# Performance work log

Measured on AMD Instinct MI355X. Metric: run time of the kernel, lower is better.

Reference implementation:

```python
import jax, jax.numpy as jnp
import numpy as np

B, T, D, H = 2, 2048, 1024, 16
DH = D // H
EPS = 1e-3  # keras LayerNormalization default epsilon


def setup_inputs() -> dict:
    key = jax.random.key(0)
    ks = jax.random.split(key, 10)
    s = 1.0 / np.sqrt(D)
    return {
        "x": jax.random.normal(ks[0], (B, T, D), jnp.float32),
        "wq": jax.random.normal(ks[1], (D, D), jnp.float32) * s,
        "bq": jnp.zeros((D,), jnp.float32),
        "wk": jax.random.normal(ks[2], (D, D), jnp.float32) * s,
        "bk": jnp.zeros((D,), jnp.float32),
        "wv": jax.random.normal(ks[3], (D, D), jnp.float32) * s,
        "bv": jnp.zeros((D,), jnp.float32),
        "wo": jax.random.normal(ks[4], (D, D), jnp.float32) * s,
        "bo": jnp.zeros((D,), jnp.float32),
        "scale": jnp.asarray(1.0, jnp.float32),  # learnable scalar, init 1.0
        "gamma": jnp.ones((D,), jnp.float32),
        "beta": jnp.zeros((D,), jnp.float32),
    }


def _split_heads(t):
    # [B,T,D] -> [B,T,H,DH] -> [H,B,T,DH]; head h takes channels h*DH:(h+1)*DH,
    # matching tf.concat(tf.split(t, H, axis=-1), axis=0) up to batch layout.
    return t.reshape(B, T, H, DH).transpose(2, 0, 1, 3)


def reference(x, wq, bq, wk, bk, wv, bv, wo, bo, scale, gamma, beta):
    q = _split_heads(x @ wq + bq)  # [H,B,T,DH]
    k = _split_heads(x @ wk + bk)
    v = _split_heads(x @ wv + bv)
    scores = scale * jnp.einsum("hbqd,hbkd->hbqk", q, k)  # [H,B,Tq,Tk]
    attn = jax.nn.softmax(scores, axis=-1)
    ctx = jnp.einsum("hbqk,hbkd->hbqd", attn, v)  # [H,B,T,DH]
    # inverse of split: heads back to last dim in head order
    merged = ctx.transpose(1, 2, 0, 3).reshape(B, T, D)
    out = merged @ wo + bo
    out = out + x  # residual connection
    mean = jnp.mean(out, axis=-1, keepdims=True)
    var = jnp.var(out, axis=-1, keepdims=True)
    out = (out - mean) * jax.lax.rsqrt(var + EPS) * gamma + beta
    return out
```

## Files before the change

kernel.cpp:

```cpp
#include <hip/hip_runtime.h>
#include <hip/hip_bf16.h>

#define B_ 2
#define T_ 2048
#define D_ 1024
#define H_ 16
#define M_ (B_ * T_)

typedef __attribute__((ext_vector_type(4))) float f32x4;
typedef __attribute__((ext_vector_type(16))) float f32x16;
typedef __attribute__((ext_vector_type(8))) short s16x8;
typedef __attribute__((ext_vector_type(4))) short s16x4;
typedef __attribute__((ext_vector_type(4))) unsigned u32x4;

__device__ __forceinline__ short f2bs(float f) {
  unsigned u = __builtin_bit_cast(unsigned, f);
  u += 0x7fffu + ((u >> 16) & 1u);
  return (short)(u >> 16);
}
__device__ __forceinline__ unsigned cvt_pk_bf16(float lo, float hi) {
  unsigned r;
  asm("v_cvt_pk_bf16_f32 %0, %1, %2" : "=v"(r) : "v"(lo), "v"(hi));
  return r;
}

__global__ __launch_bounds__(256) void cvt_f32_bf16(const float* __restrict__ in,
                                                    short* __restrict__ out, int n4) {
  int i = blockIdx.x * 256 + threadIdx.x;
  if (i < n4) {
    float4 v = ((const float4*)in)[i];
    s16x4 o;
    o.x = f2bs(v.x); o.y = f2bs(v.y); o.z = f2bs(v.z); o.w = f2bs(v.w);
    ((s16x4*)out)[i] = o;
  }
}

__global__ __launch_bounds__(256) void cvt_transpose(
    const float* __restrict__ w0, const float* __restrict__ w1,
    const float* __restrict__ w2, const float* __restrict__ w3,
    short* __restrict__ o0, short* __restrict__ o1,
    short* __restrict__ o2, short* __restrict__ o3) {
  __shared__ float tile[64][65];
  const float* W; short* Wt;
  if (blockIdx.z == 0) { W = w0; Wt = o0; }
  else if (blockIdx.z == 1) { W = w1; Wt = o1; }
  else if (blockIdx.z == 2) { W = w2; Wt = o2; }
  else { W = w3; Wt = o3; }
  const int k0 = blockIdx.x * 64, n0 = blockIdx.y * 64;
  const int t = threadIdx.x;
  const int c = t & 63, r4 = t >> 6;
#pragma unroll
  for (int i = 0; i < 16; ++i) {
    int row = i * 4 + r4;
    tile[row][c] = W[(size_t)(k0 + row) * D_ + n0 + c];
  }
  __syncthreads();
#pragma unroll
  for (int i = 0; i < 16; ++i) {
    int row = i * 4 + r4;
    Wt[(size_t)(n0 + row) * D_ + k0 + c] = f2bs(tile[c][row]);
  }
}

template <int MODE>
__device__ __forceinline__ void gemm_core(short As[128][72], short Bs[128][72],
                                          const short* __restrict__ A,
                                          const short* __restrict__ Wt,
                                          const float* __restrict__ bias,
                                          const float* __restrict__ resid,
                                          void* __restrict__ outp, float mult) {
  const int t = threadIdx.x;
  const int lane = t & 63, wid = t >> 6;
  const int l15 = lane & 15, g = lane >> 4;
  const int wr = wid >> 1, wc = wid & 1;
  const int f = blockIdx.y * 8 + blockIdx.x;
  const int nf = (f & 7) * 32 + (f >> 3);
  const int n0 = (nf & 7) * 128;
  const int m0 = (nf >> 3) * 128;

  const f32x4 fz = {0.f, 0.f, 0.f, 0.f};
  f32x4 acc[4][4];
#pragma unroll
  for (int m = 0; m < 4; ++m)
#pragma unroll
    for (int n = 0; n < 4; ++n) acc[m][n] = fz;

  const int srow = t >> 1, shalf = (t & 1) * 32;
  const short* ap = A + (size_t)(m0 + srow) * D_ + shalf;
  const short* bp = Wt + (size_t)(n0 + srow) * D_ + shalf;

  s16x8 ar[4], br[4];
#pragma unroll
  for (int c = 0; c < 4; ++c) {
    ar[c] = *(const s16x8*)(ap + c * 8);
    br[c] = *(const s16x8*)(bp + c * 8);
  }

  for (int k0 = 0; k0 < D_; k0 += 64) {
    __syncthreads();
#pragma unroll
    for (int c = 0; c < 4; ++c) {
      *(s16x8*)&As[srow][shalf + c * 8] = ar[c];
      *(s16x8*)&Bs[srow][shalf + c * 8] = br[c];
    }
    __syncthreads();
    if (k0 + 64 < D_) {
#pragma unroll
      for (int c = 0; c < 4; ++c) {
        ar[c] = *(const s16x8*)(ap + k0 + 64 + c * 8);
        br[c] = *(const s16x8*)(bp + k0 + 64 + c * 8);
      }
    }
#pragma unroll
    for (int kk = 0; kk < 64; kk += 32) {
      s16x8 af[4], bfr[4];
#pragma unroll
      for (int m = 0; m < 4; ++m)
        af[m] = *(const s16x8*)&As[wr * 64 + m * 16 + l15][kk + g * 8];
#pragma unroll
      for (int n = 0; n < 4; ++n)
        bfr[n] = *(const s16x8*)&Bs[wc * 64 + n * 16 + l15][kk + g * 8];
#pragma unroll
      for (int m = 0; m < 4; ++m)
#pragma unroll
        for (int n = 0; n < 4; ++n)
          acc[m][n] = __builtin_amdgcn_mfma_f32_16x16x32_bf16(af[m], bfr[n], acc[m][n], 0, 0, 0);
    }
  }

#pragma unroll
  for (int m = 0; m < 4; ++m) {
#pragma unroll
    for (int n = 0; n < 4; ++n) {
      const int col = n0 + wc * 64 + n * 16 + l15;
      const float bv = bias[col];
#pragma unroll
      for (int i = 0; i < 4; ++i) {
        const int row = m0 + wr * 64 + m * 16 + g * 4 + i;
        float v = acc[m][n][i] + bv;
        if (MODE == 1) {
          ((float*)outp)[(size_t)row * D_ + col] = v + resid[(size_t)row * D_ + col];
        } else {
          ((short*)outp)[(size_t)row * D_ + col] = f2bs(v * mult);
        }
      }
    }
  }
}

__global__ __launch_bounds__(256) void gemm_qkv_kernel(
    const short* __restrict__ xb, const short* __restrict__ wq,
    const short* __restrict__ wk, const short* __restrict__ wv,
    const float* __restrict__ bq, const float* __restrict__ bk,
    const float* __restrict__ bv, const float* __restrict__ scale_p,
    short* __restrict__ Qb, short* __restrict__ Kb, short* __restrict__ Vb) {
  __shared__ __align__(16) short As[128][72];
  __shared__ __align__(16) short Bs[128][72];
  const short* W;
  const float* bias;
  short* out;
  float mult = 1.0f;
  if (blockIdx.z == 0) { W = wq; bias = bq; out = Qb; mult = scale_p[0] * 1.44269504f; }
  else if (blockIdx.z == 1) { W = wk; bias = bk; out = Kb; }
  else { W = wv; bias = bv; out = Vb; }
  gemm_core<0>(As, Bs, xb, W, bias, nullptr, out, mult);
}

__global__ __launch_bounds__(256) void gemm_out_kernel(
    const short* __restrict__ ctx, const short* __restrict__ wo,
    const float* __restrict__ bo, const float* __restrict__ x,
    float* __restrict__ out) {
  __shared__ __align__(16) short As[128][72];
  __shared__ __align__(16) short Bs[128][72];
  gemm_core<1>(As, Bs, ctx, wo, bo, x, out, 1.0f);
}

__global__ __launch_bounds__(128) void attn_kernel(
    const short* __restrict__ Qb, const short* __restrict__ Kb,
    const short* __restrict__ Vb, short* __restrict__ ctx) {
  __shared__ __align__(16) short Ks[64][64];
  __shared__ __align__(16) unsigned Vt[64][36];

  const int bid = blockIdx.x;
  const int xcd = bid & 7, slot = bid >> 3;
  const int grp = ((slot >> 4) << 3) | xcd;
  const int qt = slot & 15;
  const int h = grp >> 1, b = grp & 1;

  const int hc = h * 64;
  const size_t tokbase = (size_t)b * T_;
  const int t = threadIdx.x, lane = t & 63, w = t >> 6;
  const int l31 = lane & 31, hbit = lane >> 5;
  const int swz = (l31 & 7) << 3;

  s16x8 qf[2][4];
#pragma unroll
  for (int qg = 0; qg < 2; ++qg) {
    const short* qp =
        Qb + (tokbase + (size_t)(qt * 128 + w * 64 + qg * 32 + l31)) * D_ + hc + hbit * 8;
#pragma unroll
    for (int ks = 0; ks < 4; ++ks) qf[qg][ks] = *(const s16x8*)(qp + ks * 16);
  }

  const int krow = t >> 1, kcolb = (t & 1) * 32, kswz = (krow & 7) << 3;
  const int va = t & 31, vd0 = (t >> 5) * 16;
  const short* kp = Kb + (tokbase + krow) * D_ + hc + kcolb;
  const short* vp = Vb + (tokbase + 2 * (size_t)va) * D_ + hc + vd0;

  s16x8 kr[4], vA0, vA1, vB0, vB1;
#pragma unroll
  for (int c = 0; c < 4; ++c) kr[c] = *(const s16x8*)(kp + c * 8);
  vA0 = *(const s16x8*)vp;
  vA1 = *(const s16x8*)(vp + 8);
  vB0 = *(const s16x8*)(vp + D_);
  vB1 = *(const s16x8*)(vp + D_ + 8);

  f32x16 acc[2][2];
#pragma unroll
  for (int a = 0; a < 2; ++a)
#pragma unroll
    for (int b2 = 0; b2 < 2; ++b2)
#pragma unroll
      for (int i = 0; i < 16; ++i) acc[a][b2][i] = 0.f;
  float lsum[2] = {0.f, 0.f};

  const int NT = T_ / 64;
  for (int kt = 0; kt < NT; ++kt) {
    __syncthreads();
#pragma unroll
    for (int c = 0; c < 4; ++c)
      *(s16x8*)&Ks[krow][(kcolb + c * 8) ^ kswz] = kr[c];
    {
      u32x4 a0 = __builtin_bit_cast(u32x4, vA0), b0 = __builtin_bit_cast(u32x4, vB0);
      u32x4 a1 = __builtin_bit_cast(u32x4, vA1), b1 = __builtin_bit_cast(u32x4, vB1);
#pragma unroll
      for (int jd = 0; jd < 4; ++jd) {
        Vt[vd0 + 2 * jd][va] = __builtin_amdgcn_perm(b0[jd], a0[jd], 0x05040100u);
        Vt[vd0 + 2 * jd + 1][va] = __builtin_amdgcn_perm(b0[jd], a0[jd], 0x07060302u);
        Vt[vd0 + 8 + 2 * jd][va] = __builtin_amdgcn_perm(b1[jd], a1[jd], 0x05040100u);
        Vt[vd0 + 8 + 2 * jd + 1][va] = __builtin_amdgcn_perm(b1[jd], a1[jd], 0x07060302u);
      }
    }
    __syncthreads();
    if (kt + 1 < NT) {
      const short* kp2 = kp + (size_t)(kt + 1) * 64 * D_;
#pragma unroll
      for (int c = 0; c < 4; ++c) kr[c] = *(const s16x8*)(kp2 + c * 8);
      const short* vp2 = vp + (size_t)(kt + 1) * 64 * D_;
      vA0 = *(const s16x8*)vp2;
      vA1 = *(const s16x8*)(vp2 + 8);
      vB0 = *(const s16x8*)(vp2 + D_);
      vB1 = *(const s16x8*)(vp2 + D_ + 8);
    }

#pragma unroll
    for (int kb = 0; kb < 2; ++kb) {
      s16x8 kf[4];
#pragma unroll
      for (int ks = 0; ks < 4; ++ks)
        kf[ks] = *(const s16x8*)&Ks[kb * 32 + l31][(ks * 16 + hbit * 8) ^ swz];
      f32x16 S0, S1;
#pragma unroll
      for (int i = 0; i < 16; ++i) { S0[i] = 0.f; S1[i] = 0.f; }
#pragma unroll
      for (int ks = 0; ks < 4; ++ks) {
        S0 = __builtin_amdgcn_mfma_f32_32x32x16_bf16(kf[ks], qf[0][ks], S0, 0, 0, 0);
        S1 = __builtin_amdgcn_mfma_f32_32x32x16_bf16(kf[ks], qf[1][ks], S1, 0, 0, 0);
      }
      s16x8 pf[2][2];
#pragma unroll
      for (int qg = 0; qg < 2; ++qg) {
        const f32x16& S = qg ? S1 : S0;
        unsigned d[8];
        float ls = 0.f;
#pragma unroll
        for (int m = 0; m < 4; ++m) {
          float p0 = __builtin_amdgcn_exp2f(S[4 * m + 0]);
          float p1 = __builtin_amdgcn_exp2f(S[4 * m + 1]);
          float p2 = __builtin_amdgcn_exp2f(S[4 * m + 2]);
          float p3 = __builtin_amdgcn_exp2f(S[4 * m + 3]);
          ls += (p0 + p1) + (p2 + p3);
          d[m * 2 + 0] = cvt_pk_bf16(p0, p1);
          d[m * 2 + 1] = cvt_pk_bf16(p2, p3);
        }
        lsum[qg] += ls;
#pragma unroll
        for (int s2 = 0; s2 < 2; ++s2) {
          unsigned own0 = d[(2 * s2) * 2 + 0], own1 = d[(2 * s2) * 2 + 1];
          unsigned oth0 = d[(2 * s2 + 1) * 2 + 0], oth1 = d[(2 * s2 + 1) * 2 + 1];
          unsigned send0 = hbit ? own0 : oth0;
          unsigned send1 = hbit ? own1 : oth1;
          unsigned r0 = (unsigned)__shfl_xor((int)send0, 32);
          unsigned r1 = (unsigned)__shfl_xor((int)send1, 32);
          u32x4 bf;
          bf[0] = hbit ? r0 : own0;
          bf[1] = hbit ? r1 : own1;
          bf[2] = hbit ? oth0 : r0;
          bf[3] = hbit ? oth1 : r1;
          pf[qg][s2] = __builtin_bit_cast(s16x8, bf);
        }
      }
#pragma unroll
      for (int db = 0; db < 2; ++db) {
        s16x8 av0 = *(const s16x8*)&Vt[db * 32 + l31][kb * 16 + hbit * 4];
        s16x8 av1 = *(const s16x8*)&Vt[db * 32 + l31][kb * 16 + 8 + hbit * 4];
#pragma unroll
        for (int qg = 0; qg < 2; ++qg) {
          acc[db][qg] = __builtin_amdgcn_mfma_f32_32x32x16_bf16(av0, pf[qg][0], acc[db][qg], 0, 0, 0);
          acc[db][qg] = __builtin_amdgcn_mfma_f32_32x32x16_bf16(av1, pf[qg][1], acc[db][qg], 0, 0, 0);
        }
      }
    }
  }

#pragma unroll
  for (int qg = 0; qg < 2; ++qg) {
    lsum[qg] += __shfl_xor(lsum[qg], 32);
    float inv = 1.f / lsum[qg];
    const size_t token = tokbase + (size_t)(qt * 128 + w * 64 + qg * 32 + l31);
    short* cp = ctx + token * D_ + hc;
#pragma unroll
    for (int db = 0; db < 2; ++db) {
#pragma unroll
      for (int rq = 0; rq < 4; ++rq) {
        s16x4 o;
        o.x = f2bs(acc[db][qg][rq * 4 + 0] * inv);
        o.y = f2bs(acc[db][qg][rq * 4 + 1] * inv);
        o.z = f2bs(acc[db][qg][rq * 4 + 2] * inv);
        o.w = f2bs(acc[db][qg][rq * 4 + 3] * inv);
        *(s16x4*)(cp + db * 32 + rq * 8 + hbit * 4) = o;
      }
    }
  }
}

__global__ __launch_bounds__(256) void ln_kernel(float* __restrict__ out,
                                                 const float* __restrict__ gamma,
                                                 const float* __restrict__ beta) {
  __shared__ float reds[4], redss[4];
  const size_t row = blockIdx.x;
  float* p = out + row * D_;
  const int t = threadIdx.x;
  float4 v = ((const float4*)p)[t];
  float s = v.x + v.y + v.z + v.w;
  float ss = v.x * v.x + v.y * v.y + v.z * v.z + v.w * v.w;
#pragma unroll
  for (int off = 1; off < 64; off <<= 1) {
    s += __shfl_xor(s, off);
    ss += __shfl_xor(ss, off);
  }
  const int wid = t >> 6, lane = t & 63;
  if (lane == 0) { reds[wid] = s; redss[wid] = ss; }
  __syncthreads();
  float S = reds[0] + reds[1] + reds[2] + reds[3];
  float SS = redss[0] + redss[1] + redss[2] + redss[3];
  const float mean = S * (1.f / D_);
  const float var = SS * (1.f / D_) - mean * mean;
  const float r = rsqrtf(var + 1e-3f);
  float4 gm = ((const float4*)gamma)[t];
  float4 bt = ((const float4*)beta)[t];
  float4 o;
  o.x = (v.x - mean) * r * gm.x + bt.x;
  o.y = (v.y - mean) * r * gm.y + bt.y;
  o.z = (v.z - mean) * r * gm.z + bt.z;
  o.w = (v.w - mean) * r * gm.w + bt.w;
  ((float4*)p)[t] = o;
}

extern "C" void kernel_launch(void* const* d_in, const int* in_sizes, int n_in,
                              void* d_out, int out_size, void* d_ws, size_t ws_size,
                              hipStream_t stream) {
  const float* x = (const float*)d_in[0];
  const float* wq = (const float*)d_in[1];
  const float* bq = (const float*)d_in[2];
  const float* wk = (const float*)d_in[3];
  const float* bk = (const float*)d_in[4];
  const float* wv = (const float*)d_in[5];
  const float* bv = (const float*)d_in[6];
  const float* wo = (const float*)d_in[7];
  const float* bo = (const float*)d_in[8];
  const float* scale = (const float*)d_in[9];
  const float* gamma = (const float*)d_in[10];
  const float* beta = (const float*)d_in[11];
  float* out = (float*)d_out;

  short* xb = (short*)d_ws;
  short* wqt = xb + (size_t)M_ * D_;
  short* wkt = wqt + (size_t)D_ * D_;
  short* wvt = wkt + (size_t)D_ * D_;
  short* wot = wvt + (size_t)D_ * D_;
  short* Qb = wot + (size_t)D_ * D_;
  short* Kb = Qb + (size_t)M_ * D_;
  short* Vb = Kb + (size_t)M_ * D_;
  short* ctx = Vb + (size_t)M_ * D_;

  const int n4x = M_ * D_ / 4;
  cvt_f32_bf16<<<dim3((n4x + 255) / 256), 256, 0, stream>>>(x, xb, n4x);
  cvt_transpose<<<dim3(16, 16, 4), 256, 0, stream>>>(wq, wk, wv, wo, wqt, wkt, wvt, wot);

  gemm_qkv_kernel<<<dim3(D_ / 128, M_ / 128, 3), 256, 0, stream>>>(
      xb, wqt, wkt, wvt, bq, bk, bv, scale, Qb, Kb, Vb);

  attn_kernel<<<dim3(512), 128, 0, stream>>>(Qb, Kb, Vb, ctx);

  gemm_out_kernel<<<dim3(D_ / 128, M_ / 128), 256, 0, stream>>>(ctx, wot, bo, x, out);

  ln_kernel<<<dim3(M_), 256, 0, stream>>>(out, gamma, beta);
}
```

Baseline: 134.4 us.

## Split attention KV sequence across two wave pairs and merge partial accumulators

The attention block grows from 128 to 256 threads. Each pair of waves handles one half of every 128-key chunk, staged in two shared-memory K/V buffers, so each query tile's key loop runs in half as many iterations. At the end, the second pair writes its partial output accumulators and row sums to shared memory and the first pair adds them, normalizes and stores the context. This raises wave-level parallelism per block, which matters because the grid has only 512 blocks. The cost is a larger shared-memory footprint and an extra reduction pass with two barriers, which may limit how many blocks fit per CU.

```diff
diff --git a/kernel.cpp b/kernel.cpp
--- a/kernel.cpp
+++ b/kernel.cpp
@@ -175,11 +175,14 @@
   gemm_core<1>(As, Bs, ctx, wo, bo, x, out, 1.0f);
 }
 
-__global__ __launch_bounds__(128) void attn_kernel(
+__global__ __launch_bounds__(256) void attn_kernel(
     const short* __restrict__ Qb, const short* __restrict__ Kb,
     const short* __restrict__ Vb, short* __restrict__ ctx) {
-  __shared__ __align__(16) short Ks[64][64];
-  __shared__ __align__(16) unsigned Vt[64][36];
+  __shared__ __align__(16) char smem[34816];
+  typedef short KsT[64][64];
+  typedef unsigned VtT[64][36];
+  KsT* Ks = (KsT*)smem;
+  VtT* Vt = (VtT*)(smem + 16384);
 
   const int bid = blockIdx.x;
   const int xcd = bid & 7, slot = bid >> 3;
@@ -190,6 +193,7 @@
   const int hc = h * 64;
   const size_t tokbase = (size_t)b * T_;
   const int t = threadIdx.x, lane = t & 63, w = t >> 6;
+  const int qw = w >> 1, sub = w & 1;
   const int l31 = lane & 31, hbit = lane >> 5;
   const int swz = (l31 & 7) << 3;
 
@@ -197,15 +201,16 @@
 #pragma unroll
   for (int qg = 0; qg < 2; ++qg) {
     const short* qp =
-        Qb + (tokbase + (size_t)(qt * 128 + w * 64 + qg * 32 + l31)) * D_ + hc + hbit * 8;
+        Qb + (tokbase + (size_t)(qt * 128 + qw * 64 + qg * 32 + l31)) * D_ + hc + hbit * 8;
 #pragma unroll
     for (int ks = 0; ks < 4; ++ks) qf[qg][ks] = *(const s16x8*)(qp + ks * 16);
   }
 
-  const int krow = t >> 1, kcolb = (t & 1) * 32, kswz = (krow & 7) << 3;
-  const int va = t & 31, vd0 = (t >> 5) * 16;
-  const short* kp = Kb + (tokbase + krow) * D_ + hc + kcolb;
-  const short* vp = Vb + (tokbase + 2 * (size_t)va) * D_ + hc + vd0;
+  const int th = t & 127, ts = t >> 7;
+  const int krow = th >> 1, kcolb = (th & 1) * 32, kswz = (krow & 7) << 3;
+  const int va = th & 31, vd0 = (th >> 5) * 16;
+  const short* kp = Kb + (tokbase + (size_t)(ts * 64 + krow)) * D_ + hc + kcolb;
+  const short* vp = Vb + (tokbase + (size_t)(ts * 64 + 2 * va)) * D_ + hc + vd0;
 
   s16x8 kr[4], vA0, vA1, vB0, vB1;
 #pragma unroll
@@ -224,29 +229,29 @@
       for (int i = 0; i < 16; ++i) acc[a][b2][i] = 0.f;
   float lsum[2] = {0.f, 0.f};
 
-  const int NT = T_ / 64;
-  for (int kt = 0; kt < NT; ++kt) {
+  const int NP = T_ / 128;
+  for (int j = 0; j < NP; ++j) {
     __syncthreads();
 #pragma unroll
     for (int c = 0; c < 4; ++c)
-      *(s16x8*)&Ks[krow][(kcolb + c * 8) ^ kswz] = kr[c];
+      *(s16x8*)&Ks[ts][krow][(kcolb + c * 8) ^ kswz] = kr[c];
     {
       u32x4 a0 = __builtin_bit_cast(u32x4, vA0), b0 = __builtin_bit_cast(u32x4, vB0);
       u32x4 a1 = __builtin_bit_cast(u32x4, vA1), b1 = __builtin_bit_cast(u32x4, vB1);
 #pragma unroll
       for (int jd = 0; jd < 4; ++jd) {
-        Vt[vd0 + 2 * jd][va] = __builtin_amdgcn_perm(b0[jd], a0[jd], 0x05040100u);
-        Vt[vd0 + 2 * jd + 1][va] = __builtin_amdgcn_perm(b0[jd], a0[jd], 0x07060302u);
-        Vt[vd0 + 8 + 2 * jd][va] = __builtin_amdgcn_perm(b1[jd], a1[jd], 0x05040100u);
-        Vt[vd0 + 8 + 2 * jd + 1][va] = __builtin_amdgcn_perm(b1[jd], a1[jd], 0x07060302u);
+        Vt[ts][vd0 + 2 * jd][va] = __builtin_amdgcn_perm(b0[jd], a0[jd], 0x05040100u);
+        Vt[ts][vd0 + 2 * jd + 1][va] = __builtin_amdgcn_perm(b0[jd], a0[jd], 0x07060302u);
+        Vt[ts][vd0 + 8 + 2 * jd][va] = __builtin_amdgcn_perm(b1[jd], a1[jd], 0x05040100u);
+        Vt[ts][vd0 + 8 + 2 * jd + 1][va] = __builtin_amdgcn_perm(b1[jd], a1[jd], 0x07060302u);
       }
     }
     __syncthreads();
-    if (kt + 1 < NT) {
-      const short* kp2 = kp + (size_t)(kt + 1) * 64 * D_;
+    if (j + 1 < NP) {
+      const short* kp2 = kp + (size_t)(j + 1) * 128 * D_;
 #pragma unroll
       for (int c = 0; c < 4; ++c) kr[c] = *(const s16x8*)(kp2 + c * 8);
-      const short* vp2 = vp + (size_t)(kt + 1) * 64 * D_;
+      const short* vp2 = vp + (size_t)(j + 1) * 128 * D_;
       vA0 = *(const s16x8*)vp2;
       vA1 = *(const s16x8*)(vp2 + 8);
       vB0 = *(const s16x8*)(vp2 + D_);
@@ -258,7 +263,7 @@
       s16x8 kf[4];
 #pragma unroll
       for (int ks = 0; ks < 4; ++ks)
-        kf[ks] = *(const s16x8*)&Ks[kb * 32 + l31][(ks * 16 + hbit * 8) ^ swz];
+        kf[ks] = *(const s16x8*)&Ks[sub][kb * 32 + l31][(ks * 16 + hbit * 8) ^ swz];
       f32x16 S0, S1;
 #pragma unroll
       for (int i = 0; i < 16; ++i) { S0[i] = 0.f; S1[i] = 0.f; }
@@ -302,8 +307,8 @@
       }
 #pragma unroll
       for (int db = 0; db < 2; ++db) {
-        s16x8 av0 = *(const s16x8*)&Vt[db * 32 + l31][kb * 16 + hbit * 4];
-        s16x8 av1 = *(const s16x8*)&Vt[db * 32 + l31][kb * 16 + 8 + hbit * 4];
+        s16x8 av0 = *(const s16x8*)&Vt[sub][db * 32 + l31][kb * 16 + hbit * 4];
+        s16x8 av1 = *(const s16x8*)&Vt[sub][db * 32 + l31][kb * 16 + 8 + hbit * 4];
 #pragma unroll
         for (int qg = 0; qg < 2; ++qg) {
           acc[db][qg] = __builtin_amdgcn_mfma_f32_32x32x16_bf16(av0, pf[qg][0], acc[db][qg], 0, 0, 0);
@@ -314,21 +319,48 @@
   }
 
 #pragma unroll
-  for (int qg = 0; qg < 2; ++qg) {
-    lsum[qg] += __shfl_xor(lsum[qg], 32);
-    float inv = 1.f / lsum[qg];
-    const size_t token = tokbase + (size_t)(qt * 128 + w * 64 + qg * 32 + l31);
-    short* cp = ctx + token * D_ + hc;
-#pragma unroll
-    for (int db = 0; db < 2; ++db) {
-#pragma unroll
-      for (int rq = 0; rq < 4; ++rq) {
-        s16x4 o;
-        o.x = f2bs(acc[db][qg][rq * 4 + 0] * inv);
-        o.y = f2bs(acc[db][qg][rq * 4 + 1] * inv);
-        o.z = f2bs(acc[db][qg][rq * 4 + 2] * inv);
-        o.w = f2bs(acc[db][qg][rq * 4 + 3] * inv);
-        *(s16x4*)(cp + db * 32 + rq * 8 + hbit * 4) = o;
+  for (int qg = 0; qg < 2; ++qg) lsum[qg] += __shfl_xor(lsum[qg], 32);
+
+  __syncthreads();
+  float* sh = (float*)smem;
+  if (sub == 1) {
+#pragma unroll
+    for (int qg = 0; qg < 2; ++qg) {
+#pragma unroll
+      for (int db = 0; db < 2; ++db)
+#pragma unroll
+        for (int r = 0; r < 16; ++r)
+          sh[(((qw * 2 + qg) * 2 + db) * 16 + r) * 64 + lane] = acc[db][qg][r];
+      sh[8192 + (qw * 2 + qg) * 64 + lane] = lsum[qg];
+    }
+  }
+  __syncthreads();
+  if (sub == 0) {
+#pragma unroll
+    for (int qg = 0; qg < 2; ++qg) {
+      lsum[qg] += sh[8192 + (qw * 2 + qg) * 64 + lane];
+#pragma unroll
+      for (int db = 0; db < 2; ++db)
+#pragma unroll
+        for (int r = 0; r < 16; ++r)
+          acc[db][qg][r] += sh[(((qw * 2 + qg) * 2 + db) * 16 + r) * 64 + lane];
+    }
+#pragma unroll
+    for (int qg = 0; qg < 2; ++qg) {
+      float inv = 1.f / lsum[qg];
+      const size_t token = tokbase + (size_t)(qt * 128 + qw * 64 + qg * 32 + l31);
+      short* cp = ctx + token * D_ + hc;
+#pragma unroll
+      for (int db = 0; db < 2; ++db) {
+#pragma unroll
+        for (int rq = 0; rq < 4; ++rq) {
+          s16x4 o;
+          o.x = f2bs(acc[db][qg][rq * 4 + 0] * inv);
+          o.y = f2bs(acc[db][qg][rq * 4 + 1] * inv);
+          o.z = f2bs(acc[db][qg][rq * 4 + 2] * inv);
+          o.w = f2bs(acc[db][qg][rq * 4 + 3] * inv);
+          *(s16x4*)(cp + db * 32 + rq * 8 + hbit * 4) = o;
+        }
       }
     }
   }
@@ -401,7 +433,7 @@
   gemm_qkv_kernel<<<dim3(D_ / 128, M_ / 128, 3), 256, 0, stream>>>(
       xb, wqt, wkt, wvt, bq, bk, bv, scale, Qb, Kb, Vb);
 
-  attn_kernel<<<dim3(512), 128, 0, stream>>>(Qb, Kb, Vb, ctx);
+  attn_kernel<<<dim3(512), 256, 0, stream>>>(Qb, Kb, Vb, ctx);
 
   gemm_out_kernel<<<dim3(D_ / 128, M_ / 128), 256, 0, stream>>>(ctx, wot, bo, x, out);
 
```

After: 143.4 us. 6.7% more time.

## Load GEMM tiles directly into LDS with XOR-swizzled layout

Applied to the files above, without the earlier changes.

Replaces the register-staged global loads and LDS stores in the shared GEMM core with global_load_lds direct-to-LDS transfers. The padded 72-wide LDS rows become unpadded 64-wide rows, and an XOR swizzle on the column chunk avoids bank conflicts. This cuts VGPR pressure and LDS footprint, and it removes the separate ds_write instructions. The explicit register prefetch of the next k-tile is dropped, so load latency is no longer overlapped with MFMA work within a block. That overlap must now come from other resident blocks.

```diff
diff --git a/kernel.cpp b/kernel.cpp
--- a/kernel.cpp
+++ b/kernel.cpp
@@ -22,6 +22,11 @@
   unsigned r;
   asm("v_cvt_pk_bf16_f32 %0, %1, %2" : "=v"(r) : "v"(lo), "v"(hi));
   return r;
+}
+__device__ __forceinline__ void gl_lds16(const short* g, short* l) {
+  __builtin_amdgcn_global_load_lds(
+      (const __attribute__((address_space(1))) unsigned int*)g,
+      (__attribute__((address_space(3))) unsigned int*)l, 16, 0, 0);
 }
 
 __global__ __launch_bounds__(256) void cvt_f32_bf16(const float* __restrict__ in,
@@ -63,7 +68,7 @@
 }
 
 template <int MODE>
-__device__ __forceinline__ void gemm_core(short As[128][72], short Bs[128][72],
+__device__ __forceinline__ void gemm_core(short As[128][64], short Bs[128][64],
                                           const short* __restrict__ A,
                                           const short* __restrict__ Wt,
                                           const float* __restrict__ bias,
@@ -85,41 +90,31 @@
 #pragma unroll
     for (int n = 0; n < 4; ++n) acc[m][n] = fz;
 
-  const int srow = t >> 1, shalf = (t & 1) * 32;
-  const short* ap = A + (size_t)(m0 + srow) * D_ + shalf;
-  const short* bp = Wt + (size_t)(n0 + srow) * D_ + shalf;
-
-  s16x8 ar[4], br[4];
-#pragma unroll
-  for (int c = 0; c < 4; ++c) {
-    ar[c] = *(const s16x8*)(ap + c * 8);
-    br[c] = *(const s16x8*)(bp + c * 8);
-  }
+  const int srw = lane >> 3;
+  const int csw8 = ((lane & 7) ^ srw) * 8;
+  const short* apg = A + (size_t)(m0 + wid * 32 + srw) * D_ + csw8;
+  const short* bpg = Wt + (size_t)(n0 + wid * 32 + srw) * D_ + csw8;
+
+  const int ch = ((g ^ (l15 & 7)) * 8);
 
   for (int k0 = 0; k0 < D_; k0 += 64) {
     __syncthreads();
 #pragma unroll
-    for (int c = 0; c < 4; ++c) {
-      *(s16x8*)&As[srow][shalf + c * 8] = ar[c];
-      *(s16x8*)&Bs[srow][shalf + c * 8] = br[c];
+    for (int i = 0; i < 4; ++i) {
+      gl_lds16(apg + (size_t)i * 8 * D_ + k0, &As[wid * 32 + i * 8][0]);
+      gl_lds16(bpg + (size_t)i * 8 * D_ + k0, &Bs[wid * 32 + i * 8][0]);
     }
     __syncthreads();
-    if (k0 + 64 < D_) {
-#pragma unroll
-      for (int c = 0; c < 4; ++c) {
-        ar[c] = *(const s16x8*)(ap + k0 + 64 + c * 8);
-        br[c] = *(const s16x8*)(bp + k0 + 64 + c * 8);
-      }
-    }
-#pragma unroll
-    for (int kk = 0; kk < 64; kk += 32) {
+#pragma unroll
+    for (int kk2 = 0; kk2 < 2; ++kk2) {
+      const int x = kk2 * 32;
       s16x8 af[4], bfr[4];
 #pragma unroll
       for (int m = 0; m < 4; ++m)
-        af[m] = *(const s16x8*)&As[wr * 64 + m * 16 + l15][kk + g * 8];
+        af[m] = *(const s16x8*)&As[wr * 64 + m * 16 + l15][ch ^ x];
 #pragma unroll
       for (int n = 0; n < 4; ++n)
-        bfr[n] = *(const s16x8*)&Bs[wc * 64 + n * 16 + l15][kk + g * 8];
+        bfr[n] = *(const s16x8*)&Bs[wc * 64 + n * 16 + l15][ch ^ x];
 #pragma unroll
       for (int m = 0; m < 4; ++m)
 #pragma unroll
@@ -154,8 +149,8 @@
     const float* __restrict__ bq, const float* __restrict__ bk,
     const float* __restrict__ bv, const float* __restrict__ scale_p,
     short* __restrict__ Qb, short* __restrict__ Kb, short* __restrict__ Vb) {
-  __shared__ __align__(16) short As[128][72];
-  __shared__ __align__(16) short Bs[128][72];
+  __shared__ __align__(16) short As[128][64];
+  __shared__ __align__(16) short Bs[128][64];
   const short* W;
   const float* bias;
   short* out;
@@ -170,8 +165,8 @@
     const short* __restrict__ ctx, const short* __restrict__ wo,
     const float* __restrict__ bo, const float* __restrict__ x,
     float* __restrict__ out) {
-  __shared__ __align__(16) short As[128][72];
-  __shared__ __align__(16) short Bs[128][72];
+  __shared__ __align__(16) short As[128][64];
+  __shared__ __align__(16) short Bs[128][64];
   gemm_core<1>(As, Bs, ctx, wo, bo, x, out, 1.0f);
 }
 
```

After: 137.6 us. +2.4%, slower.
